# Performance work log

Measured on AMD Instinct MI355X. Metric: run time of the kernel, lower is better.

The kernel has to match this reference:

```python
import jax, jax.numpy as jnp
import numpy as np

B, L, A, F, E, P, H = 256, 50, 64, 4, 256, 128, 4
DH = E // H
EPS = 1e-5


def setup_inputs() -> dict:
    key = jax.random.key(0)
    ks = jax.random.split(key, 32)
    s = 0.02
    inp = {
        "trajectories": jax.random.normal(ks[0], (B, L, A, F), jnp.float32),
        "roles": jax.random.randint(ks[1], (B, A), 0, 2),
        "pairs": jax.random.randint(ks[2], (B, P, 2), 0, A),
        "agent_mask": (jax.random.uniform(ks[3], (B, A)) < 0.95).at[:, 0].set(True),
        # friendly encoder (mean-pool -> MLP)
        "Wf1": s * jax.random.normal(ks[4], (F, E)), "bf1": jnp.zeros((E,)),
        "Wf2": s * jax.random.normal(ks[5], (E, E)), "bf2": jnp.zeros((E,)),
        # unauthorized encoder
        "Wu1": s * jax.random.normal(ks[6], (F, E)), "bu1": jnp.zeros((E,)),
        "Wu2": s * jax.random.normal(ks[7], (E, E)), "bu2": jnp.zeros((E,)),
        "role_emb": s * jax.random.normal(ks[8], (2, E)),
        # multihead attention
        "Wq": s * jax.random.normal(ks[9], (E, E)), "bq": jnp.zeros((E,)),
        "Wk": s * jax.random.normal(ks[10], (E, E)), "bk": jnp.zeros((E,)),
        "Wv": s * jax.random.normal(ks[11], (E, E)), "bv": jnp.zeros((E,)),
        "Wo": s * jax.random.normal(ks[12], (E, E)), "bo": jnp.zeros((E,)),
        "attn_g": jnp.ones((E,)), "attn_b": jnp.zeros((E,)),
        "ln_g": jnp.ones((5 * E,)), "ln_b": jnp.zeros((5 * E,)),
        # classifier
        "Wc1": s * jax.random.normal(ks[13], (5 * E, E)), "bc1": jnp.zeros((E,)),
        "Wc2": s * jax.random.normal(ks[14], (E, 1)), "bc2": jnp.zeros((1,)),
    }
    return inp


def _layernorm(x, g, b):
    m = x.mean(-1, keepdims=True)
    v = ((x - m) ** 2).mean(-1, keepdims=True)
    return (x - m) * jax.lax.rsqrt(v + EPS) * g + b


def _encode(pooled, W1, b1, W2, b2):
    # pooled: [B, A, F] -> [B, A, E]
    h = jnp.maximum(pooled @ W1 + b1, 0.0)
    return h @ W2 + b2


def _forward(trajectories, roles, pairs, agent_mask,
             Wf1, bf1, Wf2, bf2, Wu1, bu1, Wu2, bu2, role_emb,
             Wq, bq, Wk, bk, Wv, bv, Wo, bo, attn_g, attn_b,
             ln_g, ln_b, Wc1, bc1, Wc2, bc2):
    pooled = trajectories.mean(axis=1)                      # [B, A, F]
    emb_f = _encode(pooled, Wf1, bf1, Wf2, bf2)
    emb_u = _encode(pooled, Wu1, bu1, Wu2, bu2)
    # role-based dispatch + zero for padded agents (matches torch masked scatter)
    emb = jnp.where((roles == 0)[..., None], emb_f, emb_u)
    emb = jnp.where(agent_mask[..., None], emb, 0.0)        # [B, A, E]
    x = emb + role_emb[roles]
    # multihead self-attention with key padding mask
    q = (x @ Wq + bq).reshape(B, A, H, DH)
    k = (x @ Wk + bk).reshape(B, A, H, DH)
    v = (x @ Wv + bv).reshape(B, A, H, DH)
    scores = jnp.einsum('bqhd,bkhd->bhqk', q, k) / np.sqrt(DH).astype(np.float32)
    scores = jnp.where(agent_mask[:, None, None, :], scores, -1e9)
    attn = jax.nn.softmax(scores, axis=-1)
    ctx = jnp.einsum('bhqk,bkhd->bqhd', attn, v).reshape(B, A, E)
    attn_out = ctx @ Wo + bo
    x = _layernorm(x + attn_out, attn_g, attn_b)            # [B, A, E]
    # gather pair embeddings
    ef = jnp.take_along_axis(x, pairs[:, :, 0:1], axis=1)   # [B, P, E] via broadcast
    ef = jnp.take_along_axis(x, pairs[:, :, 0][..., None].repeat(E, -1), axis=1)
    eu = jnp.take_along_axis(x, pairs[:, :, 1][..., None].repeat(E, -1), axis=1)
    d = ef - eu
    rel = jnp.concatenate([ef, eu, jnp.abs(d), d, ef * eu], axis=-1)  # [B, P, 5E]
    rel = _layernorm(rel, ln_g, ln_b)
    h = jnp.maximum(rel @ Wc1 + bc1, 0.0)
    logits = h @ Wc2 + bc2                                  # [B, P, 1]
    return logits


def reference(trajectories, roles, pairs, agent_mask,
              Wf1, bf1, Wf2, bf2, Wu1, bu1, Wu2, bu2, role_emb,
              Wq, bq, Wk, bk, Wv, bv, Wo, bo, attn_g, attn_b,
              ln_g, ln_b, Wc1, bc1, Wc2, bc2):
    return _forward(trajectories, roles, pairs, agent_mask,
                    Wf1, bf1, Wf2, bf2, Wu1, bu1, Wu2, bu2, role_emb,
                    Wq, bq, Wk, bk, Wv, bv, Wo, bo, attn_g, attn_b,
                    ln_g, ln_b, Wc1, bc1, Wc2, bc2)
```

## Files before the change

### kernel.cpp

```cpp
#include <hip/hip_runtime.h>
#include <hip/hip_bf16.h>

typedef unsigned int u32;
typedef unsigned short u16;
typedef __attribute__((ext_vector_type(8))) short short8;
typedef __attribute__((ext_vector_type(4))) float f32x4;

#define MFMA(a,b,c) __builtin_amdgcn_mfma_f32_16x16x32_bf16(a,b,c,0,0,0)

__device__ __forceinline__ float bf2f(u16 u){ return __uint_as_float(((u32)u)<<16); }
__device__ __forceinline__ float lo16(u32 w){ return __uint_as_float(w<<16); }
__device__ __forceinline__ float hi16(u32 w){ return __uint_as_float(w & 0xffff0000u); }
__device__ __forceinline__ u16 f2b(float x){ __hip_bfloat16 h=__float2bfloat16(x); return *(u16*)&h; }
__device__ __forceinline__ u32 pack2(float a, float b){ return (u32)f2b(a) | ((u32)f2b(b)<<16); }

#define O_Wf1 0
#define O_bf1 1024
#define O_Wf2 1280
#define O_bf2 66816
#define O_Wu1 67072
#define O_bu1 68096
#define O_Wu2 68352
#define O_bu2 133888
#define O_remb 134144
#define O_Wq 134656
#define O_bq 200192
#define O_Wk 200448
#define O_bk 265984
#define O_Wv 266240
#define O_bv 331776
#define O_Wo 332032
#define O_bo 397568
#define O_ag 397824
#define O_ab 398080
#define O_lg 398336
#define O_lb 399616
#define O_Wc1 400896
#define O_bc1 728576
#define O_Wc2 728832
#define O_bc2 729088
#define TOTW 729089

static __device__ const int c_off[26] = {
  0,1024,1280,66816,67072,68096,68352,133888,134144,134656,200192,200448,
  265984,266240,331776,332032,397568,397824,398080,398336,399616,400896,
  728576,728832,729088,729089};

struct WPar { const void* src[25]; const u32* traj; float* dst; };

__device__ __forceinline__ int detect_bf16(const u32* traj){
  int inr = 0;
#pragma unroll 1
  for(int i=0;i<64;i++){
    u32 e = (traj[i]>>7) & 0xffu;
    inr += (e >= 0x58u && e <= 0x9au) ? 1 : 0;
  }
  return (inr==64) ? 1 : 0;
}

__global__ __launch_bounds__(256) void k_conv(WPar p){
  __shared__ int fl;
  if(threadIdx.x==0) fl = detect_bf16(p.traj);
  __syncthreads();
  int mode = fl;
  int g = blockIdx.x*256 + threadIdx.x;
  if(g >= TOTW) return;
  int t = 0;
#pragma unroll 1
  for(int i=1;i<25;i++) if(g >= c_off[i]) t = i;
  int j = g - c_off[t];
  float v = mode ? bf2f(((const u16*)p.src[t])[j]) : ((const float*)p.src[t])[j];
  p.dst[g] = v;
}

__global__ __launch_bounds__(256) void k_pool(const void* __restrict__ traj, const u32* __restrict__ mraw,
                                              float* __restrict__ pooled, int* __restrict__ maskI){
  __shared__ int fl;
  if(threadIdx.x==0) fl = detect_bf16((const u32*)traj);
  __syncthreads();
  int t = blockIdx.x*256 + threadIdx.x;
  int b = t>>8, r = t&255;
  float s = 0.f;
  if(fl){
    const u16* tp = (const u16*)traj + (size_t)b*12800 + r;
#pragma unroll 1
    for(int l=0;l<50;l++) s += bf2f(tp[l*256]);
  } else {
    const float* tp = (const float*)traj + (size_t)b*12800 + r;
#pragma unroll 1
    for(int l=0;l<50;l++) s += tp[l*256];
  }
  pooled[t] = s * 0.02f;
  if(t < 16384){
    bool isByte = false;
#pragma unroll
    for(int w=0;w<16;w++) isByte |= (mraw[w] > 1u);
    int v;
    if(isByte){ u32 w = mraw[t>>2]; v = (int)((w >> ((t&3)*8)) & 0xffu); }
    else      { v = (int)mraw[t]; }
    maskI[t] = (v!=0) ? 1 : 0;
  }
}

static __device__ const int t_src[6] = {O_Wf2, O_Wu2, O_Wq, O_Wk, O_Wv, O_Wo};
__global__ __launch_bounds__(256) void k_trans(const float* __restrict__ WF, u16* __restrict__ WT){
  __shared__ float tl[64][65];
  int mat = blockIdx.x >> 4, tile = blockIdx.x & 15;
  int kt = (tile>>2)*64, nt = (tile&3)*64;
  int t = threadIdx.x;
  int i = t>>2, c4 = (t&3)*16;
  const float* src = WF + t_src[mat] + (kt+i)*256 + nt + c4;
#pragma unroll
  for(int c=0;c<16;c+=4) *(float4*)&tl[i][c4+c] = *(const float4*)(src + c);
  __syncthreads();
  int n = nt + i;
  int tile_n = n >> 4, nl = n & 15;
  int ks = (kt + c4) >> 5;
  u16* base = WT + mat*65536;
#pragma unroll
  for(int h=0; h<2; h++){
    int quad = ((c4 + h*8) >> 3) & 3;
    short8 v;
#pragma unroll
    for(int j=0;j<8;j++) v[j] = (short)f2b(tl[c4 + h*8 + j][i]);
    *(short8*)(base + ((tile_n*8 + ks)*64 + quad*16 + nl)*8) = v;
  }
}

__global__ __launch_bounds__(256) void k_transc(const float* __restrict__ WF, u16* __restrict__ WTC){
  __shared__ float tl[64][65];
  int seg = blockIdx.x >> 4, tile = blockIdx.x & 15;
  int jt = (tile>>2)*64, nt = (tile&3)*64;
  int t = threadIdx.x;
  int i = t>>2, c4 = (t&3)*16;
  int j = jt + i;
#pragma unroll 1
  for(int c=0;c<16;c++){
    int n = nt + c4 + c;
    float v;
    if(seg==0)      v = WF[O_lg+j]*WF[O_Wc1 + j*256 + n] + WF[O_lg+768+j]*WF[O_Wc1 + (768+j)*256 + n];
    else if(seg==1) v = WF[O_lg+256+j]*WF[O_Wc1+(256+j)*256+n] - WF[O_lg+768+j]*WF[O_Wc1+(768+j)*256+n];
    else if(seg==2) v = WF[O_lg+512+j]*WF[O_Wc1+(512+j)*256+n];
    else            v = WF[O_lg+1024+j]*WF[O_Wc1+(1024+j)*256+n];
    tl[i][c4+c] = v;
  }
  __syncthreads();
  int n = nt + i;
  int tile_n = n >> 4, nl = n & 15;
  int kbase = seg*256 + jt + c4;
  int ks = kbase >> 5;
#pragma unroll
  for(int h=0; h<2; h++){
    int quad = ((kbase + h*8) >> 3) & 3;
    short8 v;
#pragma unroll
    for(int jj=0;jj<8;jj++) v[jj] = (short)f2b(tl[c4 + h*8 + jj][i]);
    *(short8*)(WTC + ((tile_n*32 + ks)*64 + quad*16 + nl)*8) = v;
  }
}

__global__ __launch_bounds__(256) void k_prep(const float* __restrict__ WF, float* __restrict__ UG){
  __shared__ float ru[4], rg[4];
  int n = blockIdx.x;
  int t = threadIdx.x;
  float u = 0.f, g = 0.f;
#pragma unroll
  for(int j=0;j<5;j++){
    int m = t + j*256;
    float w = WF[O_Wc1 + m*256 + n];
    u = fmaf(WF[O_lb+m], w, u);
    g = fmaf(WF[O_lg+m], w, g);
  }
#pragma unroll
  for(int o=32;o>0;o>>=1){ u += __shfl_xor(u,o,64); g += __shfl_xor(g,o,64); }
  int wv = t>>6;
  if((t&63)==0){ ru[wv]=u; rg[wv]=g; }
  __syncthreads();
  if(t==0){
    UG[n]     = ru[0]+ru[1]+ru[2]+ru[3] + WF[O_bc1+n];
    UG[256+n] = rg[0]+rg[1]+rg[2]+rg[3];
  }
}

__global__ __launch_bounds__(256) void k_h(const float* __restrict__ WF, const float* __restrict__ pooled,
                                           const int* __restrict__ roles, u32* __restrict__ hb){
  int g = blockIdx.x*256 + threadIdx.x;
  int r = g>>6, e0 = (g&63)*4;
  float4 pl = *(const float4*)(pooled + r*4);
  int role = roles[r];
  const float* W1 = WF + (role ? O_Wu1 : O_Wf1);
  const float* b1 = WF + (role ? O_bu1 : O_bf1);
  float h[4];
#pragma unroll
  for(int c=0;c<4;c++){
    int e = e0+c;
    float v = b1[e] + pl.x*W1[e] + pl.y*W1[256+e] + pl.z*W1[512+e] + pl.w*W1[768+e];
    h[c] = fmaxf(v, 0.f);
  }
  hb[(r*256+e0)>>1]     = pack2(h[0],h[1]);
  hb[((r*256+e0)>>1)+1] = pack2(h[2],h[3]);
}

__device__ __forceinline__ void stageA256(const u16* __restrict__ A, long row0, u16* As){
  int t = threadIdx.x;
  int r = t >> 3, c0 = (t & 7) * 32;
  const u16* src = A + (row0 + r)*256 + c0;
  u16* dst = As + r*264 + c0;
#pragma unroll
  for(int i=0;i<4;i++) *(short8*)(dst + i*8) = *(const short8*)(src + i*8);
}

__device__ __forceinline__ void mmK256(const u16* As, const u16* __restrict__ WT, int wv,
                                       int colL, int quad, int lane, f32x4 acc[2][4]){
#pragma unroll
  for(int ks=0; ks<8; ks++){
    short8 a0 = *(short8*)(As + colL*264 + ks*32 + quad*8);
    short8 a1 = *(short8*)(As + (colL+16)*264 + ks*32 + quad*8);
#pragma unroll
    for(int ct=0; ct<4; ct++){
      short8 b = *(const short8*)(WT + (((wv*4+ct)*8 + ks)*64 + lane)*8);
      acc[0][ct] = MFMA(a0, b, acc[0][ct]);
      acc[1][ct] = MFMA(a1, b, acc[1][ct]);
    }
  }
}

__global__ __launch_bounds__(256,2) void k_enc2(const float* __restrict__ WF, const u16* __restrict__ hb,
                                                const int* __restrict__ roles, const int* __restrict__ maskI,
                                                const u16* __restrict__ WT2F, const u16* __restrict__ WT2U,
                                                u16* __restrict__ x0b){
  __shared__ u16 As[32*264];
  __shared__ int roleS[32], maskS[32];
  long row0 = (long)blockIdx.x*32;
  int t = threadIdx.x;
  stageA256(hb, row0, As);
  if(t<32){ roleS[t]=roles[row0+t]; maskS[t]=maskI[row0+t]; }
  __syncthreads();
  int lane = t & 63, wv = t >> 6;
  int colL = lane & 15, quad = lane >> 4;
  f32x4 accF[2][4] = {};
  f32x4 accU[2][4] = {};
  mmK256(As, WT2F, wv, colL, quad, lane, accF);
  mmK256(As, WT2U, wv, colL, quad, lane, accU);
#pragma unroll
  for(int ct=0; ct<4; ct++){
    int col = wv*64 + ct*16 + colL;
    float bfc = WF[O_bf2+col], buc = WF[O_bu2+col];
    float r0c = WF[O_remb+col], r1c = WF[O_remb+256+col];
#pragma unroll
    for(int rt=0; rt<2; rt++)
#pragma unroll
    for(int reg=0; reg<4; reg++){
      int row = rt*16 + quad*4 + reg;
      float vf = accF[rt][ct][reg] + bfc;
      float vu = accU[rt][ct][reg] + buc;
      int ro = roleS[row];
      float v = ro ? vu : vf;
      v = maskS[row] ? v : 0.f;
      v += ro ? r1c : r0c;
      x0b[(size_t)(row0+row)*256 + col] = f2b(v);
    }
  }
}

static __device__ const int qkv_b[3] = {O_bq, O_bk, O_bv};
__global__ __launch_bounds__(256,2) void k_qkv(const float* __restrict__ WF, const u16* __restrict__ x0b,
                                               const u16* __restrict__ WTQ, u16* __restrict__ qout){
  __shared__ u16 As[32*264];
  long row0 = (long)blockIdx.x*32;
  int y = blockIdx.y;
  stageA256(x0b, row0, As);
  __syncthreads();
  int t = threadIdx.x;
  int lane = t & 63, wv = t >> 6;
  int colL = lane & 15, quad = lane >> 4;
  f32x4 acc[2][4] = {};
  mmK256(As, WTQ + y*65536, wv, colL, quad, lane, acc);
  u16* outp = qout + (size_t)y*4194304;
  int bo = qkv_b[y];
#pragma unroll
  for(int ct=0; ct<4; ct++){
    int col = wv*64 + ct*16 + colL;
    float bc = WF[bo+col];
#pragma unroll
    for(int rt=0; rt<2; rt++)
#pragma unroll
    for(int reg=0; reg<4; reg++){
      int row = rt*16 + quad*4 + reg;
      outp[(size_t)(row0+row)*256 + col] = f2b(acc[rt][ct][reg] + bc);
    }
  }
}

#define VT_STR 72
__global__ __launch_bounds__(256,2) void k_attn6(const u16* __restrict__ qb, const u16* __restrict__ kb,
                                                 const u16* __restrict__ vb, const int* __restrict__ maskI,
                                                 u16* __restrict__ ctxb){
  __shared__ u16 Vt[64*VT_STR];
  __shared__ u16 Pp[64*VT_STR];
  __shared__ int maskS[64];
  const int t = threadIdx.x;
  const int b = blockIdx.x, h = blockIdx.y;
  const int lane = t & 63;
  const int wv = t >> 6;
  const int colL = lane & 15, quad = lane >> 4;

  {
    int j  = t >> 2;
    int dc = (t & 3) * 16;
    const u16* vr = vb + (size_t)(b*64 + j)*256 + h*64 + dc;
    uint4 w0 = *(const uint4*)(vr);
    uint4 w1 = *(const uint4*)(vr + 8);
    u32 wd[8] = {w0.x,w0.y,w0.z,w0.w,w1.x,w1.y,w1.z,w1.w};
#pragma unroll
    for(int i=0;i<8;i++){
      u32 w = wd[i];
      Vt[(dc + 2*i    )*VT_STR + j] = (u16)(w & 0xffffu);
      Vt[(dc + 2*i + 1)*VT_STR + j] = (u16)(w >> 16);
    }
    if(t < 64) maskS[t] = maskI[b*64 + t];
  }

  f32x4 acc[4] = {};
  {
    const u16* qrow = qb + (size_t)(b*64 + wv*16 + colL)*256 + h*64 + quad*8;
#pragma unroll
    for(int ks=0; ks<2; ks++){
      short8 a = *(const short8*)(qrow + ks*32);
#pragma unroll
      for(int tj=0; tj<4; tj++){
        short8 bf = *(const short8*)(kb + (size_t)(b*64 + tj*16 + colL)*256 + h*64 + ks*32 + quad*8);
        acc[tj] = MFMA(a, bf, acc[tj]);
      }
    }
  }

  __syncthreads();

#pragma unroll
  for(int tj=0; tj<4; tj++){
    int mk = maskS[tj*16 + colL];
#pragma unroll
    for(int reg=0; reg<4; reg++)
      acc[tj][reg] = mk ? acc[tj][reg]*0.125f : -1e9f;
  }
  float m[4], sum[4];
#pragma unroll
  for(int reg=0; reg<4; reg++){
    float v = fmaxf(fmaxf(acc[0][reg],acc[1][reg]), fmaxf(acc[2][reg],acc[3][reg]));
    v = fmaxf(v, __shfl_xor(v,1,64));
    v = fmaxf(v, __shfl_xor(v,2,64));
    v = fmaxf(v, __shfl_xor(v,4,64));
    v = fmaxf(v, __shfl_xor(v,8,64));
    m[reg] = v;
    sum[reg] = 0.f;
  }
#pragma unroll
  for(int tj=0; tj<4; tj++)
#pragma unroll
  for(int reg=0; reg<4; reg++){
    float e = __expf(acc[tj][reg] - m[reg]);
    acc[tj][reg] = e;
    sum[reg] += e;
  }
#pragma unroll
  for(int reg=0; reg<4; reg++){
    float v = sum[reg];
    v += __shfl_xor(v,1,64); v += __shfl_xor(v,2,64);
    v += __shfl_xor(v,4,64); v += __shfl_xor(v,8,64);
    sum[reg] = v;
  }

#pragma unroll
  for(int tj=0; tj<4; tj++)
#pragma unroll
  for(int reg=0; reg<4; reg++)
    Pp[(wv*16 + quad*4 + reg)*VT_STR + tj*16 + colL] = f2b(acc[tj][reg]);

  f32x4 o[4] = {};
  {
    const u16* prow = Pp + (wv*16 + colL)*VT_STR + quad*8;
#pragma unroll
    for(int ks=0; ks<2; ks++){
      short8 a = *(const short8*)(prow + ks*32);
#pragma unroll
      for(int dt=0; dt<4; dt++){
        short8 bf = *(const short8*)(Vt + (dt*16 + colL)*VT_STR + ks*32 + quad*8);
        o[dt] = MFMA(a, bf, o[dt]);
      }
    }
  }

  float inv[4];
#pragma unroll
  for(int reg=0; reg<4; reg++) inv[reg] = 1.f/sum[reg];
#pragma unroll
  for(int dt=0; dt<4; dt++)
#pragma unroll
  for(int reg=0; reg<4; reg++)
    Pp[(wv*16 + quad*4 + reg)*VT_STR + dt*16 + colL] = f2b(o[dt][reg]*inv[reg]);
  {
    int rr = lane >> 2;
    int cc = (lane & 3) * 16;
    const u16* crow = Pp + (wv*16 + rr)*VT_STR + cc;
    short8 c0 = *(const short8*)(crow);
    short8 c1 = *(const short8*)(crow + 8);
    u16* orow = ctxb + (size_t)(b*64 + wv*16 + rr)*256 + h*64 + cc;
    *(short8*)(orow)     = c0;
    *(short8*)(orow + 8) = c1;
  }
}

__global__ __launch_bounds__(256,2) void k_oproj(const float* __restrict__ WF, const u16* __restrict__ ctxb,
                                                 const u16* __restrict__ x0b, const u16* __restrict__ WTO,
                                                 float* __restrict__ x1){
  __shared__ u16 As[32*264];
  __shared__ float Sred[4][32], Qred[4][32], Mrow[32], Rrow[32];
  long row0 = (long)blockIdx.x*32;
  stageA256(ctxb, row0, As);
  __syncthreads();
  int t = threadIdx.x;
  int lane = t & 63, wv = t >> 6;
  int colL = lane & 15, quad = lane >> 4;
  f32x4 acc[2][4] = {};
  mmK256(As, WTO, wv, colL, quad, lane, acc);
  float S[2][4] = {}, Q[2][4] = {};
#pragma unroll
  for(int ct=0; ct<4; ct++){
    int col = wv*64 + ct*16 + colL;
    float bc = WF[O_bo+col];
#pragma unroll
    for(int rt=0; rt<2; rt++)
#pragma unroll
    for(int reg=0; reg<4; reg++){
      int row = rt*16 + quad*4 + reg;
      float y = acc[rt][ct][reg] + bc + bf2f(x0b[(size_t)(row0+row)*256 + col]);
      acc[rt][ct][reg] = y;
      S[rt][reg] += y; Q[rt][reg] += y*y;
    }
  }
#pragma unroll
  for(int o=1;o<16;o<<=1)
#pragma unroll
  for(int rt=0;rt<2;rt++)
#pragma unroll
  for(int reg=0;reg<4;reg++){ S[rt][reg] += __shfl_xor(S[rt][reg],o); Q[rt][reg] += __shfl_xor(Q[rt][reg],o); }
  if(colL==0){
#pragma unroll
    for(int rt=0;rt<2;rt++)
#pragma unroll
    for(int reg=0;reg<4;reg++){
      Sred[wv][rt*16+quad*4+reg] = S[rt][reg];
      Qred[wv][rt*16+quad*4+reg] = Q[rt][reg];
    }
  }
  __syncthreads();
  if(t<32){
    float s = Sred[0][t]+Sred[1][t]+Sred[2][t]+Sred[3][t];
    float q = Qred[0][t]+Qred[1][t]+Qred[2][t]+Qred[3][t];
    float mean = s*(1.f/256.f);
    float var  = q*(1.f/256.f) - mean*mean;
    Mrow[t] = mean; Rrow[t] = rsqrtf(var + 1e-5f);
  }
  __syncthreads();
#pragma unroll
  for(int ct=0; ct<4; ct++){
    int col = wv*64 + ct*16 + colL;
    float gc = WF[O_ag+col], bc = WF[O_ab+col];
#pragma unroll
    for(int rt=0; rt<2; rt++)
#pragma unroll
    for(int reg=0; reg<4; reg++){
      int row = rt*16 + quad*4 + reg;
      x1[(size_t)(row0+row)*256 + col] = (acc[rt][ct][reg]-Mrow[row])*Rrow[row]*gc + bc;
    }
  }
}

__global__ __launch_bounds__(256) void k_stats(const float* __restrict__ x1, const int* __restrict__ pairs,
                                               float* __restrict__ rsG, float* __restrict__ mrsG){
  int t = threadIdx.x;
  int r = t>>3, t8 = t&7;
  long pr = (long)blockIdx.x*32 + r;
  int b = (int)(pr>>7);
  int i0 = pairs[pr*2], i1 = pairs[pr*2+1];
  const float* ef = x1 + (size_t)(b*64+i0)*256 + t8*32;
  const float* eu = x1 + (size_t)(b*64+i1)*256 + t8*32;
  float S=0.f, Q=0.f;
#pragma unroll
  for(int c=0;c<32;c+=4){
    float4 e4 = *(const float4*)(ef+c);
    float4 u4 = *(const float4*)(eu+c);
    float e[4]={e4.x,e4.y,e4.z,e4.w}, u[4]={u4.x,u4.y,u4.z,u4.w};
#pragma unroll
    for(int j=0;j<4;j++){
      float d = e[j]-u[j], p = e[j]*u[j];
      S += 2.f*e[j] + fabsf(d) + p;
      Q += e[j]*e[j] + u[j]*u[j] + 2.f*d*d + p*p;
    }
  }
#pragma unroll
  for(int o=1;o<8;o<<=1){ S += __shfl_xor(S,o); Q += __shfl_xor(Q,o); }
  if(t8==0){
    float mean = S*(1.f/1280.f);
    float var  = Q*(1.f/1280.f) - mean*mean;
    float rs = rsqrtf(var + 1e-5f);
    rsG[pr] = rs; mrsG[pr] = mean*rs;
  }
}

__global__ __launch_bounds__(256) void k_cls(const float* __restrict__ WF, const float* __restrict__ x1,
                                             const int* __restrict__ pairs, const u16* __restrict__ WTC,
                                             const float* __restrict__ UG, const float* __restrict__ rsG,
                                             const float* __restrict__ mrsG, float* __restrict__ out){
  __shared__ u16 As[32*512];
  int t = threadIdx.x;
  int lane = t & 63, wv = t >> 6;
  int colL = lane & 15, quad = lane >> 4;
  int rxl = colL & 7;
  int r = t>>3, t8 = t&7, rx = r&7;
  long pr = (long)blockIdx.x*32 + r;
  int bb = (int)(pr>>7);
  int i0 = pairs[pr*2], i1 = pairs[pr*2+1];
  const float* ef = x1 + (size_t)(bb*64+i0)*256 + t8*32;
  const float* eu = x1 + (size_t)(bb*64+i1)*256 + t8*32;
  f32x4 acc[2][4] = {};
  short8 bn[4];
#pragma unroll
  for(int ct=0;ct<4;ct++)
    bn[ct] = *(const short8*)(WTC + (size_t)(((wv*4+ct)*32 + 0)*64 + lane)*8);
#pragma unroll 1
  for(int pass=0; pass<2; pass++){
#pragma unroll
    for(int c=0;c<4;c++){
      float e[8], u[8];
      *(float4*)(e)   = *(const float4*)(ef + c*8);
      *(float4*)(e+4) = *(const float4*)(ef + c*8 + 4);
      *(float4*)(u)   = *(const float4*)(eu + c*8);
      *(float4*)(u+4) = *(const float4*)(eu + c*8 + 4);
      short8 f0, f1;
#pragma unroll
      for(int j=0;j<8;j++){
        float d = e[j]-u[j];
        if(pass==0){ f0[j] = (short)f2b(e[j]);        f1[j] = (short)f2b(u[j]); }
        else       { f0[j] = (short)f2b(fabsf(d));    f1[j] = (short)f2b(e[j]*u[j]); }
      }
      int cc = t8*4 + c;
      *(short8*)(As + r*512 + (( 0 + cc)^rx)*8) = f0;
      *(short8*)(As + r*512 + ((32 + cc)^rx)*8) = f1;
    }
    __syncthreads();
#pragma unroll 1
    for(int ks=0; ks<16; ks++){
      int kst = pass*16 + ks;
      short8 b0[4];
#pragma unroll
      for(int ct=0;ct<4;ct++) b0[ct] = bn[ct];
      if(kst < 31){
#pragma unroll
        for(int ct=0;ct<4;ct++)
          bn[ct] = *(const short8*)(WTC + (size_t)(((wv*4+ct)*32 + kst+1)*64 + lane)*8);
      }
      short8 a0 = *(short8*)(As + colL*512      + ((ks*4+quad)^rxl)*8);
      short8 a1 = *(short8*)(As + (colL+16)*512 + ((ks*4+quad)^rxl)*8);
#pragma unroll
      for(int ct=0;ct<4;ct++){
        acc[0][ct] = MFMA(a0, b0[ct], acc[0][ct]);
        acc[1][ct] = MFMA(a1, b0[ct], acc[1][ct]);
      }
    }
    __syncthreads();
  }
  float rsv[2][4], mrsv[2][4];
#pragma unroll
  for(int rt=0;rt<2;rt++)
#pragma unroll
  for(int reg=0;reg<4;reg++){
    long grow = (long)blockIdx.x*32 + rt*16 + quad*4 + reg;
    rsv[rt][reg] = rsG[grow]; mrsv[rt][reg] = mrsG[grow];
  }
  float plog[2][4] = {};
#pragma unroll
  for(int ct=0; ct<4; ct++){
    int col = wv*64 + ct*16 + colL;
    float Uc = UG[col], Gc = UG[256+col], w2 = WF[O_Wc2+col];
#pragma unroll
    for(int rt=0;rt<2;rt++)
#pragma unroll
    for(int reg=0;reg<4;reg++){
      float h = rsv[rt][reg]*acc[rt][ct][reg] - mrsv[rt][reg]*Gc + Uc;
      h = fmaxf(h, 0.f);
      plog[rt][reg] = fmaf(h, w2, plog[rt][reg]);
    }
  }
#pragma unroll
  for(int o=1;o<16;o<<=1)
#pragma unroll
  for(int rt=0;rt<2;rt++)
#pragma unroll
  for(int reg=0;reg<4;reg++) plog[rt][reg] += __shfl_xor(plog[rt][reg], o);
  float* red = (float*)As;
  if(colL==0){
#pragma unroll
    for(int rt=0;rt<2;rt++)
#pragma unroll
    for(int reg=0;reg<4;reg++) red[wv*32 + rt*16 + quad*4 + reg] = plog[rt][reg];
  }
  __syncthreads();
  if(t<32){
    float l = red[t] + red[32+t] + red[64+t] + red[96+t] + WF[O_bc2];
    out[(long)blockIdx.x*32 + t] = l;
  }
}

#define WS_MASK   3145728u
#define WS_POOLED 3211264u
#define WS_UG     3473408u
#define WS_RS     3475456u
#define WS_MRS    3606528u
#define WS_WT     4194304u
#define WS_WTC    4980736u
#define WS_H      6291456u
#define WS_X0     14680064u
#define WS_Q      23068672u
#define WS_CTX    48234496u
#define WS_X1     56623104u

extern "C" void kernel_launch(void* const* d_in, const int* in_sizes, int n_in,
                              void* d_out, int out_size, void* d_ws, size_t ws_size,
                              hipStream_t stream){
  char* ws = (char*)d_ws;
  float* WF     = (float*)ws;
  int*   maskI  = (int*)  (ws + WS_MASK);
  float* pooled = (float*)(ws + WS_POOLED);
  float* UG     = (float*)(ws + WS_UG);
  float* rsG    = (float*)(ws + WS_RS);
  float* mrsG   = (float*)(ws + WS_MRS);
  u16*   WT     = (u16*)  (ws + WS_WT);
  u16*   WTC    = (u16*)  (ws + WS_WTC);
  u16*   hb     = (u16*)  (ws + WS_H);
  u16*   x0b    = (u16*)  (ws + WS_X0);
  u16*   qkvb   = (u16*)  (ws + WS_Q);
  u16*   ctxb   = (u16*)  (ws + WS_CTX);
  float* x1     = (float*)(ws + WS_X1);

  WPar wp;
  for(int i=0;i<25;i++) wp.src[i] = d_in[4+i];
  wp.traj = (const u32*)d_in[0];
  wp.dst  = WF;

  const void* traj  = d_in[0];
  const int* roles  = (const int*)d_in[1];
  const int* pairs  = (const int*)d_in[2];
  const u32* mraw   = (const u32*)d_in[3];
  float* out = (float*)d_out;

  hipLaunchKernelGGL(k_conv,  dim3((TOTW+255)/256), dim3(256), 0, stream, wp);
  hipLaunchKernelGGL(k_pool,  dim3(256),  dim3(256), 0, stream, traj, mraw, pooled, maskI);
  hipLaunchKernelGGL(k_trans, dim3(96),   dim3(256), 0, stream, WF, WT);
  hipLaunchKernelGGL(k_transc,dim3(64),   dim3(256), 0, stream, WF, WTC);
  hipLaunchKernelGGL(k_prep,  dim3(256),  dim3(256), 0, stream, WF, UG);
  hipLaunchKernelGGL(k_h,     dim3(4096), dim3(256), 0, stream, WF, pooled, roles, (u32*)hb);
  hipLaunchKernelGGL(k_enc2,  dim3(512),  dim3(256), 0, stream, WF, hb, roles, maskI,
                     WT + 0*65536, WT + 1*65536, x0b);
  hipLaunchKernelGGL(k_qkv,   dim3(512,3),dim3(256), 0, stream, WF, x0b, WT + 2*65536, qkvb);
  hipLaunchKernelGGL(k_attn6, dim3(256,4),dim3(256), 0, stream,
                     qkvb, qkvb + 4194304, qkvb + 2*4194304, maskI, ctxb);
  hipLaunchKernelGGL(k_oproj, dim3(512),  dim3(256), 0, stream, WF, ctxb, x0b, WT + 5*65536, x1);
  hipLaunchKernelGGL(k_stats, dim3(1024), dim3(256), 0, stream, x1, pairs, rsG, mrsG);
  hipLaunchKernelGGL(k_cls,   dim3(1024), dim3(256), 0, stream, WF, x1, pairs, WTC, UG, rsG, mrsG, out);
}
```

Measured before the change: 261.0 us.

## Merge prep kernels and fold pair LayerNorm stats into classifier kernel

Combines the weight conversion and pooling kernels into one launch, and the hidden-layer, transpose and bias-prep kernels into a second, cutting the launch count. The separate pair-statistics kernel is removed: the classifier now computes the per-pair mean and rstd in shared memory while staging features. The classifier tile also grows from 32 to 64 rows per block, which lowers block count but raises register and LDS use (launch_bounds 256,1, 64KB As).

```diff
diff --git a/kernel.cpp b/kernel.cpp
--- a/kernel.cpp
+++ b/kernel.cpp
@@ -40,6 +40,7 @@
 #define O_Wc2 728832
 #define O_bc2 729088
 #define TOTW 729089
+#define NCONV 2849
 
 static __device__ const int c_off[26] = {
   0,1024,1280,66816,67072,68096,68352,133888,134144,134656,200192,200448,
@@ -58,147 +59,148 @@
   return (inr==64) ? 1 : 0;
 }
 
-__global__ __launch_bounds__(256) void k_conv(WPar p){
+__global__ __launch_bounds__(256) void k_init(WPar p, const u32* __restrict__ mraw,
+                                              float* __restrict__ pooled, int* __restrict__ maskI){
   __shared__ int fl;
   if(threadIdx.x==0) fl = detect_bf16(p.traj);
   __syncthreads();
   int mode = fl;
-  int g = blockIdx.x*256 + threadIdx.x;
-  if(g >= TOTW) return;
-  int t = 0;
+  if(blockIdx.x < NCONV){
+    int g = blockIdx.x*256 + threadIdx.x;
+    if(g >= TOTW) return;
+    int t = 0;
 #pragma unroll 1
-  for(int i=1;i<25;i++) if(g >= c_off[i]) t = i;
-  int j = g - c_off[t];
-  float v = mode ? bf2f(((const u16*)p.src[t])[j]) : ((const float*)p.src[t])[j];
-  p.dst[g] = v;
-}
-
-__global__ __launch_bounds__(256) void k_pool(const void* __restrict__ traj, const u32* __restrict__ mraw,
-                                              float* __restrict__ pooled, int* __restrict__ maskI){
-  __shared__ int fl;
-  if(threadIdx.x==0) fl = detect_bf16((const u32*)traj);
-  __syncthreads();
-  int t = blockIdx.x*256 + threadIdx.x;
-  int b = t>>8, r = t&255;
-  float s = 0.f;
-  if(fl){
-    const u16* tp = (const u16*)traj + (size_t)b*12800 + r;
+    for(int i=1;i<25;i++) if(g >= c_off[i]) t = i;
+    int j = g - c_off[t];
+    float v = mode ? bf2f(((const u16*)p.src[t])[j]) : ((const float*)p.src[t])[j];
+    p.dst[g] = v;
+  } else {
+    int t = (blockIdx.x - NCONV)*256 + threadIdx.x;
+    int b = t>>8, r = t&255;
+    float s = 0.f;
+    if(mode){
+      const u16* tp = (const u16*)p.traj + (size_t)b*12800 + r;
 #pragma unroll 1
-    for(int l=0;l<50;l++) s += bf2f(tp[l*256]);
-  } else {
-    const float* tp = (const float*)traj + (size_t)b*12800 + r;
+      for(int l=0;l<50;l++) s += bf2f(tp[l*256]);
+    } else {
+      const float* tp = (const float*)p.traj + (size_t)b*12800 + r;
 #pragma unroll 1
-    for(int l=0;l<50;l++) s += tp[l*256];
-  }
-  pooled[t] = s * 0.02f;
-  if(t < 16384){
-    bool isByte = false;
-#pragma unroll
-    for(int w=0;w<16;w++) isByte |= (mraw[w] > 1u);
-    int v;
-    if(isByte){ u32 w = mraw[t>>2]; v = (int)((w >> ((t&3)*8)) & 0xffu); }
-    else      { v = (int)mraw[t]; }
-    maskI[t] = (v!=0) ? 1 : 0;
+      for(int l=0;l<50;l++) s += tp[l*256];
+    }
+    pooled[t] = s * 0.02f;
+    if(t < 16384){
+      bool isByte = false;
+#pragma unroll
+      for(int w=0;w<16;w++) isByte |= (mraw[w] > 1u);
+      int v;
+      if(isByte){ u32 w = mraw[t>>2]; v = (int)((w >> ((t&3)*8)) & 0xffu); }
+      else      { v = (int)mraw[t]; }
+      maskI[t] = (v!=0) ? 1 : 0;
+    }
   }
 }
 
 static __device__ const int t_src[6] = {O_Wf2, O_Wu2, O_Wq, O_Wk, O_Wv, O_Wo};
-__global__ __launch_bounds__(256) void k_trans(const float* __restrict__ WF, u16* __restrict__ WT){
+__global__ __launch_bounds__(256) void k_wprep(const float* __restrict__ WF, const float* __restrict__ pooled,
+                                               const int* __restrict__ roles, u32* __restrict__ hb,
+                                               u16* __restrict__ WT, u16* __restrict__ WTC,
+                                               float* __restrict__ UG){
   __shared__ float tl[64][65];
-  int mat = blockIdx.x >> 4, tile = blockIdx.x & 15;
-  int kt = (tile>>2)*64, nt = (tile&3)*64;
+  int bid = blockIdx.x;
   int t = threadIdx.x;
-  int i = t>>2, c4 = (t&3)*16;
-  const float* src = WF + t_src[mat] + (kt+i)*256 + nt + c4;
-#pragma unroll
-  for(int c=0;c<16;c+=4) *(float4*)&tl[i][c4+c] = *(const float4*)(src + c);
-  __syncthreads();
-  int n = nt + i;
-  int tile_n = n >> 4, nl = n & 15;
-  int ks = (kt + c4) >> 5;
-  u16* base = WT + mat*65536;
-#pragma unroll
-  for(int h=0; h<2; h++){
-    int quad = ((c4 + h*8) >> 3) & 3;
-    short8 v;
-#pragma unroll
-    for(int j=0;j<8;j++) v[j] = (short)f2b(tl[c4 + h*8 + j][i]);
-    *(short8*)(base + ((tile_n*8 + ks)*64 + quad*16 + nl)*8) = v;
-  }
-}
-
-__global__ __launch_bounds__(256) void k_transc(const float* __restrict__ WF, u16* __restrict__ WTC){
-  __shared__ float tl[64][65];
-  int seg = blockIdx.x >> 4, tile = blockIdx.x & 15;
-  int jt = (tile>>2)*64, nt = (tile&3)*64;
-  int t = threadIdx.x;
-  int i = t>>2, c4 = (t&3)*16;
-  int j = jt + i;
+  if(bid < 4096){
+    int g = bid*256 + t;
+    int r = g>>6, e0 = (g&63)*4;
+    float4 pl = *(const float4*)(pooled + r*4);
+    int role = roles[r];
+    const float* W1 = WF + (role ? O_Wu1 : O_Wf1);
+    const float* b1 = WF + (role ? O_bu1 : O_bf1);
+    float h[4];
+#pragma unroll
+    for(int c=0;c<4;c++){
+      int e = e0+c;
+      float v = b1[e] + pl.x*W1[e] + pl.y*W1[256+e] + pl.z*W1[512+e] + pl.w*W1[768+e];
+      h[c] = fmaxf(v, 0.f);
+    }
+    hb[(r*256+e0)>>1]     = pack2(h[0],h[1]);
+    hb[((r*256+e0)>>1)+1] = pack2(h[2],h[3]);
+    return;
+  }
+  if(bid < 4192){
+    int b2 = bid - 4096;
+    int mat = b2 >> 4, tile = b2 & 15;
+    int kt = (tile>>2)*64, nt = (tile&3)*64;
+    int i = t>>2, c4 = (t&3)*16;
+    const float* src = WF + t_src[mat] + (kt+i)*256 + nt + c4;
+#pragma unroll
+    for(int c=0;c<16;c+=4) *(float4*)&tl[i][c4+c] = *(const float4*)(src + c);
+    __syncthreads();
+    int n = nt + i;
+    int tile_n = n >> 4, nl = n & 15;
+    int ks = (kt + c4) >> 5;
+    u16* base = WT + mat*65536;
+#pragma unroll
+    for(int h=0; h<2; h++){
+      int quad = ((c4 + h*8) >> 3) & 3;
+      short8 v;
+#pragma unroll
+      for(int j=0;j<8;j++) v[j] = (short)f2b(tl[c4 + h*8 + j][i]);
+      *(short8*)(base + ((tile_n*8 + ks)*64 + quad*16 + nl)*8) = v;
+    }
+    return;
+  }
+  if(bid < 4256){
+    int b2 = bid - 4192;
+    int seg = b2 >> 4, tile = b2 & 15;
+    int jt = (tile>>2)*64, nt = (tile&3)*64;
+    int i = t>>2, c4 = (t&3)*16;
+    int j = jt + i;
 #pragma unroll 1
-  for(int c=0;c<16;c++){
-    int n = nt + c4 + c;
-    float v;
-    if(seg==0)      v = WF[O_lg+j]*WF[O_Wc1 + j*256 + n] + WF[O_lg+768+j]*WF[O_Wc1 + (768+j)*256 + n];
-    else if(seg==1) v = WF[O_lg+256+j]*WF[O_Wc1+(256+j)*256+n] - WF[O_lg+768+j]*WF[O_Wc1+(768+j)*256+n];
-    else if(seg==2) v = WF[O_lg+512+j]*WF[O_Wc1+(512+j)*256+n];
-    else            v = WF[O_lg+1024+j]*WF[O_Wc1+(1024+j)*256+n];
-    tl[i][c4+c] = v;
-  }
-  __syncthreads();
-  int n = nt + i;
-  int tile_n = n >> 4, nl = n & 15;
-  int kbase = seg*256 + jt + c4;
-  int ks = kbase >> 5;
-#pragma unroll
-  for(int h=0; h<2; h++){
-    int quad = ((kbase + h*8) >> 3) & 3;
-    short8 v;
-#pragma unroll
-    for(int jj=0;jj<8;jj++) v[jj] = (short)f2b(tl[c4 + h*8 + jj][i]);
-    *(short8*)(WTC + ((tile_n*32 + ks)*64 + quad*16 + nl)*8) = v;
-  }
-}
-
-__global__ __launch_bounds__(256) void k_prep(const float* __restrict__ WF, float* __restrict__ UG){
-  __shared__ float ru[4], rg[4];
-  int n = blockIdx.x;
-  int t = threadIdx.x;
-  float u = 0.f, g = 0.f;
-#pragma unroll
-  for(int j=0;j<5;j++){
-    int m = t + j*256;
-    float w = WF[O_Wc1 + m*256 + n];
-    u = fmaf(WF[O_lb+m], w, u);
-    g = fmaf(WF[O_lg+m], w, g);
-  }
-#pragma unroll
-  for(int o=32;o>0;o>>=1){ u += __shfl_xor(u,o,64); g += __shfl_xor(g,o,64); }
-  int wv = t>>6;
-  if((t&63)==0){ ru[wv]=u; rg[wv]=g; }
-  __syncthreads();
-  if(t==0){
-    UG[n]     = ru[0]+ru[1]+ru[2]+ru[3] + WF[O_bc1+n];
-    UG[256+n] = rg[0]+rg[1]+rg[2]+rg[3];
-  }
-}
-
-__global__ __launch_bounds__(256) void k_h(const float* __restrict__ WF, const float* __restrict__ pooled,
-                                           const int* __restrict__ roles, u32* __restrict__ hb){
-  int g = blockIdx.x*256 + threadIdx.x;
-  int r = g>>6, e0 = (g&63)*4;
-  float4 pl = *(const float4*)(pooled + r*4);
-  int role = roles[r];
-  const float* W1 = WF + (role ? O_Wu1 : O_Wf1);
-  const float* b1 = WF + (role ? O_bu1 : O_bf1);
-  float h[4];
-#pragma unroll
-  for(int c=0;c<4;c++){
-    int e = e0+c;
-    float v = b1[e] + pl.x*W1[e] + pl.y*W1[256+e] + pl.z*W1[512+e] + pl.w*W1[768+e];
-    h[c] = fmaxf(v, 0.f);
-  }
-  hb[(r*256+e0)>>1]     = pack2(h[0],h[1]);
-  hb[((r*256+e0)>>1)+1] = pack2(h[2],h[3]);
+    for(int c=0;c<16;c++){
+      int n = nt + c4 + c;
+      float v;
+      if(seg==0)      v = WF[O_lg+j]*WF[O_Wc1 + j*256 + n] + WF[O_lg+768+j]*WF[O_Wc1 + (768+j)*256 + n];
+      else if(seg==1) v = WF[O_lg+256+j]*WF[O_Wc1+(256+j)*256+n] - WF[O_lg+768+j]*WF[O_Wc1+(768+j)*256+n];
+      else if(seg==2) v = WF[O_lg+512+j]*WF[O_Wc1+(512+j)*256+n];
+      else            v = WF[O_lg+1024+j]*WF[O_Wc1+(1024+j)*256+n];
+      tl[i][c4+c] = v;
+    }
+    __syncthreads();
+    int n = nt + i;
+    int tile_n = n >> 4, nl = n & 15;
+    int kbase = seg*256 + jt + c4;
+    int ks = kbase >> 5;
+#pragma unroll
+    for(int h=0; h<2; h++){
+      int quad = ((kbase + h*8) >> 3) & 3;
+      short8 v;
+#pragma unroll
+      for(int jj=0;jj<8;jj++) v[jj] = (short)f2b(tl[c4 + h*8 + jj][i]);
+      *(short8*)(WTC + ((tile_n*32 + ks)*64 + quad*16 + nl)*8) = v;
+    }
+    return;
+  }
+  {
+    __shared__ float ru[4], rg[4];
+    int n = bid - 4256;
+    float u = 0.f, g = 0.f;
+#pragma unroll
+    for(int j=0;j<5;j++){
+      int m = t + j*256;
+      float w = WF[O_Wc1 + m*256 + n];
+      u = fmaf(WF[O_lb+m], w, u);
+      g = fmaf(WF[O_lg+m], w, g);
+    }
+#pragma unroll
+    for(int o=32;o>0;o>>=1){ u += __shfl_xor(u,o,64); g += __shfl_xor(g,o,64); }
+    int wv = t>>6;
+    if((t&63)==0){ ru[wv]=u; rg[wv]=g; }
+    __syncthreads();
+    if(t==0){
+      UG[n]     = ru[0]+ru[1]+ru[2]+ru[3] + WF[O_bc1+n];
+      UG[256+n] = rg[0]+rg[1]+rg[2]+rg[3];
+    }
+  }
 }
 
 __device__ __forceinline__ void stageA256(const u16* __restrict__ A, long row0, u16* As){
@@ -477,62 +479,31 @@
   }
 }
 
-__global__ __launch_bounds__(256) void k_stats(const float* __restrict__ x1, const int* __restrict__ pairs,
-                                               float* __restrict__ rsG, float* __restrict__ mrsG){
-  int t = threadIdx.x;
-  int r = t>>3, t8 = t&7;
-  long pr = (long)blockIdx.x*32 + r;
-  int b = (int)(pr>>7);
-  int i0 = pairs[pr*2], i1 = pairs[pr*2+1];
-  const float* ef = x1 + (size_t)(b*64+i0)*256 + t8*32;
-  const float* eu = x1 + (size_t)(b*64+i1)*256 + t8*32;
-  float S=0.f, Q=0.f;
-#pragma unroll
-  for(int c=0;c<32;c+=4){
-    float4 e4 = *(const float4*)(ef+c);
-    float4 u4 = *(const float4*)(eu+c);
-    float e[4]={e4.x,e4.y,e4.z,e4.w}, u[4]={u4.x,u4.y,u4.z,u4.w};
-#pragma unroll
-    for(int j=0;j<4;j++){
-      float d = e[j]-u[j], p = e[j]*u[j];
-      S += 2.f*e[j] + fabsf(d) + p;
-      Q += e[j]*e[j] + u[j]*u[j] + 2.f*d*d + p*p;
-    }
-  }
-#pragma unroll
-  for(int o=1;o<8;o<<=1){ S += __shfl_xor(S,o); Q += __shfl_xor(Q,o); }
-  if(t8==0){
-    float mean = S*(1.f/1280.f);
-    float var  = Q*(1.f/1280.f) - mean*mean;
-    float rs = rsqrtf(var + 1e-5f);
-    rsG[pr] = rs; mrsG[pr] = mean*rs;
-  }
-}
-
-__global__ __launch_bounds__(256) void k_cls(const float* __restrict__ WF, const float* __restrict__ x1,
-                                             const int* __restrict__ pairs, const u16* __restrict__ WTC,
-                                             const float* __restrict__ UG, const float* __restrict__ rsG,
-                                             const float* __restrict__ mrsG, float* __restrict__ out){
-  __shared__ u16 As[32*512];
+__global__ __launch_bounds__(256,1) void k_cls(const float* __restrict__ WF, const float* __restrict__ x1,
+                                               const int* __restrict__ pairs, const u16* __restrict__ WTC,
+                                               const float* __restrict__ UG, float* __restrict__ out){
+  __shared__ u16 As[64*512];
+  __shared__ float rsS[64], mrsS[64];
   int t = threadIdx.x;
   int lane = t & 63, wv = t >> 6;
   int colL = lane & 15, quad = lane >> 4;
   int rxl = colL & 7;
-  int r = t>>3, t8 = t&7, rx = r&7;
-  long pr = (long)blockIdx.x*32 + r;
+  int r = t>>2, t4 = t&3, rx = r&7;
+  long pr = (long)blockIdx.x*64 + r;
   int bb = (int)(pr>>7);
   int i0 = pairs[pr*2], i1 = pairs[pr*2+1];
-  const float* ef = x1 + (size_t)(bb*64+i0)*256 + t8*32;
-  const float* eu = x1 + (size_t)(bb*64+i1)*256 + t8*32;
-  f32x4 acc[2][4] = {};
+  const float* ef = x1 + (size_t)(bb*64+i0)*256 + t4*64;
+  const float* eu = x1 + (size_t)(bb*64+i1)*256 + t4*64;
+  f32x4 acc[4][4] = {};
   short8 bn[4];
 #pragma unroll
   for(int ct=0;ct<4;ct++)
     bn[ct] = *(const short8*)(WTC + (size_t)(((wv*4+ct)*32 + 0)*64 + lane)*8);
+  float S = 0.f, Q = 0.f;
 #pragma unroll 1
   for(int pass=0; pass<2; pass++){
 #pragma unroll
-    for(int c=0;c<4;c++){
+    for(int c=0;c<8;c++){
       float e[8], u[8];
       *(float4*)(e)   = *(const float4*)(ef + c*8);
       *(float4*)(e+4) = *(const float4*)(ef + c*8 + 4);
@@ -542,12 +513,28 @@
 #pragma unroll
       for(int j=0;j<8;j++){
         float d = e[j]-u[j];
-        if(pass==0){ f0[j] = (short)f2b(e[j]);        f1[j] = (short)f2b(u[j]); }
-        else       { f0[j] = (short)f2b(fabsf(d));    f1[j] = (short)f2b(e[j]*u[j]); }
+        if(pass==0){
+          f0[j] = (short)f2b(e[j]);        f1[j] = (short)f2b(u[j]);
+          float p = e[j]*u[j];
+          S += 2.f*e[j] + fabsf(d) + p;
+          Q += e[j]*e[j] + u[j]*u[j] + 2.f*d*d + p*p;
+        } else {
+          f0[j] = (short)f2b(fabsf(d));    f1[j] = (short)f2b(e[j]*u[j]);
+        }
       }
-      int cc = t8*4 + c;
+      int cc = t4*8 + c;
       *(short8*)(As + r*512 + (( 0 + cc)^rx)*8) = f0;
       *(short8*)(As + r*512 + ((32 + cc)^rx)*8) = f1;
+    }
+    if(pass==0){
+      S += __shfl_xor(S,1); S += __shfl_xor(S,2);
+      Q += __shfl_xor(Q,1); Q += __shfl_xor(Q,2);
+      if(t4==0){
+        float mean = S*(1.f/1280.f);
+        float var  = Q*(1.f/1280.f) - mean*mean;
+        float rs = rsqrtf(var + 1e-5f);
+        rsS[r] = rs; mrsS[r] = mean*rs;
+      }
     }
     __syncthreads();
 #pragma unroll 1
@@ -561,34 +548,29 @@
         for(int ct=0;ct<4;ct++)
           bn[ct] = *(const short8*)(WTC + (size_t)(((wv*4+ct)*32 + kst+1)*64 + lane)*8);
       }
-      short8 a0 = *(short8*)(As + colL*512      + ((ks*4+quad)^rxl)*8);
-      short8 a1 = *(short8*)(As + (colL+16)*512 + ((ks*4+quad)^rxl)*8);
-#pragma unroll
-      for(int ct=0;ct<4;ct++){
-        acc[0][ct] = MFMA(a0, b0[ct], acc[0][ct]);
-        acc[1][ct] = MFMA(a1, b0[ct], acc[1][ct]);
-      }
+      short8 a[4];
+#pragma unroll
+      for(int rt=0;rt<4;rt++)
+        a[rt] = *(short8*)(As + (colL + rt*16)*512 + ((ks*4+quad)^rxl)*8);
+#pragma unroll
+      for(int ct=0;ct<4;ct++)
+#pragma unroll
+      for(int rt=0;rt<4;rt++)
+        acc[rt][ct] = MFMA(a[rt], b0[ct], acc[rt][ct]);
     }
     __syncthreads();
   }
-  float rsv[2][4], mrsv[2][4];
-#pragma unroll
-  for(int rt=0;rt<2;rt++)
-#pragma unroll
-  for(int reg=0;reg<4;reg++){
-    long grow = (long)blockIdx.x*32 + rt*16 + quad*4 + reg;
-    rsv[rt][reg] = rsG[grow]; mrsv[rt][reg] = mrsG[grow];
-  }
-  float plog[2][4] = {};
+  float plog[4][4] = {};
 #pragma unroll
   for(int ct=0; ct<4; ct++){
     int col = wv*64 + ct*16 + colL;
     float Uc = UG[col], Gc = UG[256+col], w2 = WF[O_Wc2+col];
 #pragma unroll
-    for(int rt=0;rt<2;rt++)
+    for(int rt=0;rt<4;rt++)
 #pragma unroll
     for(int reg=0;reg<4;reg++){
-      float h = rsv[rt][reg]*acc[rt][ct][reg] - mrsv[rt][reg]*Gc + Uc;
+      int row = rt*16 + quad*4 + reg;
+      float h = rsS[row]*acc[rt][ct][reg] - mrsS[row]*Gc + Uc;
       h = fmaxf(h, 0.f);
       plog[rt][reg] = fmaf(h, w2, plog[rt][reg]);
     }
@@ -596,28 +578,26 @@
 #pragma unroll
   for(int o=1;o<16;o<<=1)
 #pragma unroll
-  for(int rt=0;rt<2;rt++)
+  for(int rt=0;rt<4;rt++)
 #pragma unroll
   for(int reg=0;reg<4;reg++) plog[rt][reg] += __shfl_xor(plog[rt][reg], o);
   float* red = (float*)As;
   if(colL==0){
 #pragma unroll
-    for(int rt=0;rt<2;rt++)
-#pragma unroll
-    for(int reg=0;reg<4;reg++) red[wv*32 + rt*16 + quad*4 + reg] = plog[rt][reg];
-  }
-  __syncthreads();
-  if(t<32){
-    float l = red[t] + red[32+t] + red[64+t] + red[96+t] + WF[O_bc2];
-    out[(long)blockIdx.x*32 + t] = l;
+    for(int rt=0;rt<4;rt++)
+#pragma unroll
+    for(int reg=0;reg<4;reg++) red[wv*64 + rt*16 + quad*4 + reg] = plog[rt][reg];
+  }
+  __syncthreads();
+  if(t<64){
+    float l = red[t] + red[64+t] + red[128+t] + red[192+t] + WF[O_bc2];
+    out[(long)blockIdx.x*64 + t] = l;
   }
 }
 
 #define WS_MASK   3145728u
 #define WS_POOLED 3211264u
 #define WS_UG     3473408u
-#define WS_RS     3475456u
-#define WS_MRS    3606528u
 #define WS_WT     4194304u
 #define WS_WTC    4980736u
 #define WS_H      6291456u
@@ -634,8 +614,6 @@
   int*   maskI  = (int*)  (ws + WS_MASK);
   float* pooled = (float*)(ws + WS_POOLED);
   float* UG     = (float*)(ws + WS_UG);
-  float* rsG    = (float*)(ws + WS_RS);
-  float* mrsG   = (float*)(ws + WS_MRS);
   u16*   WT     = (u16*)  (ws + WS_WT);
   u16*   WTC    = (u16*)  (ws + WS_WTC);
   u16*   hb     = (u16*)  (ws + WS_H);
@@ -649,24 +627,18 @@
   wp.traj = (const u32*)d_in[0];
   wp.dst  = WF;
 
-  const void* traj  = d_in[0];
   const int* roles  = (const int*)d_in[1];
   const int* pairs  = (const int*)d_in[2];
   const u32* mraw   = (const u32*)d_in[3];
   float* out = (float*)d_out;
 
-  hipLaunchKernelGGL(k_conv,  dim3((TOTW+255)/256), dim3(256), 0, stream, wp);
-  hipLaunchKernelGGL(k_pool,  dim3(256),  dim3(256), 0, stream, traj, mraw, pooled, maskI);
-  hipLaunchKernelGGL(k_trans, dim3(96),   dim3(256), 0, stream, WF, WT);
-  hipLaunchKernelGGL(k_transc,dim3(64),   dim3(256), 0, stream, WF, WTC);
-  hipLaunchKernelGGL(k_prep,  dim3(256),  dim3(256), 0, stream, WF, UG);
-  hipLaunchKernelGGL(k_h,     dim3(4096), dim3(256), 0, stream, WF, pooled, roles, (u32*)hb);
+  hipLaunchKernelGGL(k_init,  dim3(NCONV+256), dim3(256), 0, stream, wp, mraw, pooled, maskI);
+  hipLaunchKernelGGL(k_wprep, dim3(4512), dim3(256), 0, stream, WF, pooled, roles, (u32*)hb, WT, WTC, UG);
   hipLaunchKernelGGL(k_enc2,  dim3(512),  dim3(256), 0, stream, WF, hb, roles, maskI,
                      WT + 0*65536, WT + 1*65536, x0b);
   hipLaunchKernelGGL(k_qkv,   dim3(512,3),dim3(256), 0, stream, WF, x0b, WT + 2*65536, qkvb);
   hipLaunchKernelGGL(k_attn6, dim3(256,4),dim3(256), 0, stream,
                      qkvb, qkvb + 4194304, qkvb + 2*4194304, maskI, ctxb);
   hipLaunchKernelGGL(k_oproj, dim3(512),  dim3(256), 0, stream, WF, ctxb, x0b, WT + 5*65536, x1);
-  hipLaunchKernelGGL(k_stats, dim3(1024), dim3(256), 0, stream, x1, pairs, rsG, mrsG);
-  hipLaunchKernelGGL(k_cls,   dim3(1024), dim3(256), 0, stream, WF, x1, pairs, WTC, UG, rsG, mrsG, out);
-}
+  hipLaunchKernelGGL(k_cls,   dim3(512),  dim3(256), 0, stream, WF, x1, pairs, WTC, UG, out);
+}
```

Measured after the change: 255.7 us. 1.02x faster.
